# Optimization experiments

Measured on AMD Instinct MI355X. Metric: run time of the kernel, lower is better.

## Reference

```python
import jax, jax.numpy as jnp
import numpy as np

B, S, H = 2, 2048, 2048
HEADS, G = 16, 4
HD = H // HEADS          # 128
M = HEADS // G           # query heads per KV group


def setup_inputs() -> dict:
    key = jax.random.key(0)
    ks = jax.random.split(key, 6)
    s = 0.02
    hidden_state = jax.random.normal(ks[0], (B, S, H), dtype=jnp.float32)
    attention_mask = jnp.ones((B, 1, 1, S), dtype=jnp.float32)
    Wq = jax.random.normal(ks[1], (H, H), dtype=jnp.float32) * s
    bq = jnp.zeros((H,), dtype=jnp.float32)
    Wk = jax.random.normal(ks[2], (H, G * HD), dtype=jnp.float32) * s
    bk = jnp.zeros((G * HD,), dtype=jnp.float32)
    Wv = jax.random.normal(ks[3], (H, G * HD), dtype=jnp.float32) * s
    bv = jnp.zeros((G * HD,), dtype=jnp.float32)
    Wo = jax.random.normal(ks[4], (H, H), dtype=jnp.float32) * s
    bo = jnp.zeros((H,), dtype=jnp.float32)
    return {"hidden_state": hidden_state, "attention_mask": attention_mask,
            "Wq": Wq, "bq": bq, "Wk": Wk, "bk": bk, "Wv": Wv, "bv": bv,
            "Wo": Wo, "bo": bo}


def reference(hidden_state, attention_mask, Wq, bq, Wk, bk, Wv, bv, Wo, bo):
    b, s, h = hidden_state.shape
    # projections
    q = hidden_state @ Wq + bq                      # (B,S,H)
    k = hidden_state @ Wk + bk                      # (B,S,G*HD)
    v = hidden_state @ Wv + bv                      # (B,S,G*HD)
    # split heads; query head ordering is group-major (head = g*M + m),
    # matching the original expand/reshape of K/V groups.
    q = q.reshape(b, s, HEADS, HD).transpose(0, 2, 1, 3).reshape(b, G, M, s, HD)
    k = k.reshape(b, s, G, HD).transpose(0, 2, 1, 3)  # (B,G,S,HD)
    v = v.reshape(b, s, G, HD).transpose(0, 2, 1, 3)  # (B,G,S,HD)
    # grouped attention: avoid materializing expanded K/V
    scale = 1.0 / jnp.sqrt(jnp.float32(HD))
    scores = jnp.einsum('bgmqd,bgkd->bgmqk', q, k) * scale  # (B,G,M,S,S)
    # faithful to source: scores += mask * -1e-9 (mask shape (B,1,1,S))
    scores = scores + attention_mask[:, :, :, None, :] * (-1e-9)
    probs = jax.nn.softmax(scores, axis=-1)
    out = jnp.einsum('bgmqk,bgkd->bgmqd', probs, v)          # (B,G,M,S,HD)
    out = out.reshape(b, HEADS, s, HD).transpose(0, 2, 1, 3).reshape(b, s, h)
    return out @ Wo + bo
```

## Files before the change

kernel.cpp:

```cpp
#include <hip/hip_runtime.h>
#include <cstdint>

typedef unsigned short u16;
typedef __attribute__((ext_vector_type(8))) short bf16x8;
typedef __attribute__((ext_vector_type(4))) float f32x4;

#define B_    2
#define S_    2048
#define H_    2048
#define G_    4
#define HD_   128
#define QKVW  3072

#define EXP2F(x) __builtin_amdgcn_exp2f(x)

__device__ __forceinline__ u16 f2bf(float f) {
  union { float f; unsigned u; } v; v.f = f;
  unsigned r = v.u + 0x7fffu + ((v.u >> 16) & 1u);
  return (u16)(r >> 16);
}

__device__ __forceinline__ void async16(void* lds_dst, const void* gsrc) {
  __builtin_amdgcn_global_load_lds(
      (__attribute__((address_space(1))) void*)gsrc,
      (__attribute__((address_space(3))) void*)lds_dst, 16, 0, 0);
}

__global__ __launch_bounds__(256)
void prelude_kernel(const float* __restrict__ X, u16* __restrict__ Xb,
                    const float* __restrict__ Wq, const float* __restrict__ Wk,
                    const float* __restrict__ Wv, const float* __restrict__ Wo,
                    u16* __restrict__ Wqkvt, u16* __restrict__ Wot)
{
  int id = blockIdx.x;
  if (id < 4096) {
    int i = id * 256 + threadIdx.x;
    const float4* p = (const float4*)X + (size_t)i * 2;
    float4 a = p[0], b = p[1];
    u16 h[8] = { f2bf(a.x), f2bf(a.y), f2bf(a.z), f2bf(a.w),
                 f2bf(b.x), f2bf(b.y), f2bf(b.z), f2bf(b.w) };
    *(uint4*)(Xb + (size_t)i * 8) = *(const uint4*)h;
    return;
  }
  id -= 4096;
  const float* W; u16* Wt; int Ndim, bx;
  if (id < 4096)      { W = Wq; Wt = Wqkvt;                        Ndim = 2048; bx = id;        }
  else if (id < 5120) { W = Wk; Wt = Wqkvt + (size_t)2048 * 2048;  Ndim = 512;  bx = id - 4096; }
  else if (id < 6144) { W = Wv; Wt = Wqkvt + (size_t)2560 * 2048;  Ndim = 512;  bx = id - 5120; }
  else                { W = Wo; Wt = Wot;                          Ndim = 2048; bx = id - 6144; }
  const int Kdim = 2048;
  const int nbx = Ndim >> 5;
  const int n0 = (bx % nbx) * 32, k0 = (bx / nbx) * 32;

  __shared__ float t[32][33];
  int tx = threadIdx.x & 31, ty = threadIdx.x >> 5;
#pragma unroll
  for (int j = 0; j < 4; ++j)
    t[ty + j * 8][tx] = W[(size_t)(k0 + ty + j * 8) * Ndim + n0 + tx];
  __syncthreads();
#pragma unroll
  for (int j = 0; j < 4; ++j)
    Wt[(size_t)(n0 + ty + j * 8) * Kdim + k0 + tx] = f2bf(t[tx][ty + j * 8]);
}

__global__ __launch_bounds__(256)
void vtrans_kernel(const u16* __restrict__ Vb, u16* __restrict__ Vt)
{
  __shared__ u16 t[32][33];
  int tx = threadIdx.x & 31, ty = threadIdx.x >> 5;
  int s0 = blockIdx.x * 32, c0 = blockIdx.y * 32, b = blockIdx.z;
#pragma unroll
  for (int j = 0; j < 4; ++j)
    t[ty + j * 8][tx] = Vb[((size_t)(b * S_) + s0 + ty + j * 8) * QKVW + c0 + tx];
  __syncthreads();
#pragma unroll
  for (int j = 0; j < 4; ++j) {
    int c = c0 + ty + j * 8;
    int g = c >> 7, d = c & 127;
    Vt[(((size_t)(b * G_ + g)) * HD_ + d) * S_ + s0 + tx] = t[tx][ty + j * 8];
  }
}

template <int MODE>
__global__ __launch_bounds__(512, 6)
void gemm_bt(const u16* __restrict__ A, const u16* __restrict__ Bt,
             const float* __restrict__ biasQ, const float* __restrict__ biasK,
             const float* __restrict__ biasV, void* __restrict__ Cout,
             int Ndim, int Kdim)
{
  __shared__ u16 As[128 * 64];
  __shared__ u16 Bs[128 * 64];
  const int tid  = threadIdx.x;
  const int lane = tid & 63;
  const int wv   = tid >> 6;

  const int nwg  = gridDim.x * gridDim.y;
  const int wgid = blockIdx.x + gridDim.x * blockIdx.y;
  const int cpx  = nwg >> 3;
  const int swz  = (wgid & 7) * cpx + (wgid >> 3);
  const int row0 = (swz % gridDim.x) * 128;
  const int col0 = (swz / gridDim.x) * 128;

  const int wm = (wv >> 2) * 64;
  const int wn = (wv & 3) * 32;
  const int l15 = lane & 15, l4 = lane >> 4;

  f32x4 acc[4][2] = {};

  for (int kt = 0; kt < Kdim; kt += 64) {
    __syncthreads();
#pragma unroll
    for (int i = 0; i < 2; ++i) {
      int u = i * 512 + tid;
      int r = u >> 3, ci = u & 7;
      async16((char*)As + (i * 512 + wv * 64) * 16,
              A + (size_t)(row0 + r) * Kdim + kt + ci * 8);
    }
#pragma unroll
    for (int i = 0; i < 2; ++i) {
      int u = i * 512 + tid;
      int r = u >> 3, ci = u & 7;
      async16((char*)Bs + (i * 512 + wv * 64) * 16,
              Bt + (size_t)(col0 + r) * Kdim + kt + ci * 8);
    }
    __syncthreads();
#pragma unroll
    for (int ks = 0; ks < 2; ++ks) {
      bf16x8 af[4], bfr[2];
#pragma unroll
      for (int mt = 0; mt < 4; ++mt)
        af[mt] = *(const bf16x8*)&As[(wm + mt * 16 + l15) * 64 + ks * 32 + l4 * 8];
#pragma unroll
      for (int nt = 0; nt < 2; ++nt)
        bfr[nt] = *(const bf16x8*)&Bs[(wn + nt * 16 + l15) * 64 + ks * 32 + l4 * 8];
#pragma unroll
      for (int mt = 0; mt < 4; ++mt)
#pragma unroll
        for (int nt = 0; nt < 2; ++nt)
          acc[mt][nt] = __builtin_amdgcn_mfma_f32_16x16x32_bf16(af[mt], bfr[nt], acc[mt][nt], 0, 0, 0);
    }
  }

#pragma unroll
  for (int mt = 0; mt < 4; ++mt)
#pragma unroll
    for (int nt = 0; nt < 2; ++nt)
#pragma unroll
      for (int r = 0; r < 4; ++r) {
        int rr = row0 + wm + mt * 16 + l4 * 4 + r;
        int cc = col0 + wn + nt * 16 + l15;
        float bias;
        if (MODE == 3)
          bias = cc < 2048 ? biasQ[cc] : (cc < 2560 ? biasK[cc - 2048] : biasV[cc - 2560]);
        else
          bias = biasQ[cc];
        float v = acc[mt][nt][r] + bias;
        if (MODE == 3 && cc < 2048) v *= 0.12751743383412927f;
        if (MODE == 1) ((float*)Cout)[(size_t)rr * Ndim + cc] = v;
        else           ((u16*)Cout)[(size_t)rr * Ndim + cc] = f2bf(v);
      }
}

__global__ __launch_bounds__(512, 2)
void attn_kernel(const u16* __restrict__ Qb, const u16* __restrict__ Kb,
                 const u16* __restrict__ Vt, u16* __restrict__ Ob)
{
  __shared__ u16 SH[40960];
  u16* Ps = SH + 24576;
  const int tid  = threadIdx.x;
  const int lane = tid & 63, wv = tid >> 6;
  const int l15 = lane & 15, l4 = lane >> 4;
  const int qt = blockIdx.x, head = blockIdx.y, b = blockIdx.z;
  const int g = head >> 2;
  const int s0 = qt * 256;

  bf16x8 qf[2][4];
  {
    const u16* qbase = Qb + ((size_t)(b * S_ + s0 + wv * 32 + l15)) * QKVW + head * HD_ + l4 * 8;
#pragma unroll
    for (int rg = 0; rg < 2; ++rg)
#pragma unroll
      for (int ks = 0; ks < 4; ++ks)
        qf[rg][ks] = *(const bf16x8*)(qbase + (size_t)rg * 16 * QKVW + ks * 32);
  }

  float m_r[2][4], lp[2][4];
#pragma unroll
  for (int rg = 0; rg < 2; ++rg)
#pragma unroll
    for (int r = 0; r < 4; ++r) { m_r[rg][r] = 0.f; lp[rg][r] = 0.f; }
  f32x4 aco[2][8] = {};

#define STAGE_K(buf, kt_)                                                      \
  _Pragma("unroll")                                                            \
  for (int i = 0; i < 2; ++i) {                                                \
    int u = i * 512 + tid;                                                     \
    int r = u >> 4;                                                            \
    int ci = (u & 15) ^ (r & 7);                                               \
    async16((char*)SH + (buf) * 16384 + (i * 512 + wv * 64) * 16,              \
            Kb + ((size_t)(b * S_ + (kt_) * 64 + r)) * QKVW + g * HD_ + ci * 8); \
  }
#define STAGE_V(kt_)                                                           \
  _Pragma("unroll")                                                            \
  for (int i = 0; i < 2; ++i) {                                                \
    int u = i * 512 + tid;                                                     \
    int r = u >> 3;                                                            \
    int ci = (u & 7) ^ (r & 7);                                                \
    async16((char*)SH + 32768 + (i * 512 + wv * 64) * 16,                      \
            Vt + (((size_t)(b * G_ + g)) * HD_ + r) * S_ + (kt_) * 64 + ci * 8); \
  }

  STAGE_K(0, 0);
  STAGE_V(0);
  __syncthreads();

  const u16* Vc = SH + 16384;
  int kcur = 0;
  for (int kt = 0; kt < S_ / 64; ++kt) {
    if (kt + 1 < S_ / 64) {
      STAGE_K(kcur ^ 1, kt + 1);
    }
    const u16* Kc = SH + kcur * 8192;

    f32x4 sc[2][4] = {};
    __builtin_amdgcn_s_setprio(1);
#pragma unroll
    for (int ct = 0; ct < 4; ++ct)
#pragma unroll
      for (int ks = 0; ks < 4; ++ks) {
        bf16x8 kf = *(const bf16x8*)&Kc[(ct * 16 + l15) * 128 + ((ks * 32 + l4 * 8) ^ ((l15 & 7) << 3))];
        sc[0][ct] = __builtin_amdgcn_mfma_f32_16x16x32_bf16(qf[0][ks], kf, sc[0][ct], 0, 0, 0);
        sc[1][ct] = __builtin_amdgcn_mfma_f32_16x16x32_bf16(qf[1][ks], kf, sc[1][ct], 0, 0, 0);
      }
    __builtin_amdgcn_s_setprio(0);

    float lm[2][4];
    bool resc = false;
#pragma unroll
    for (int rg = 0; rg < 2; ++rg)
#pragma unroll
      for (int r = 0; r < 4; ++r) {
        lm[rg][r] = fmaxf(fmaxf(sc[rg][0][r], sc[rg][1][r]),
                          fmaxf(sc[rg][2][r], sc[rg][3][r]));
        float d = lm[rg][r] - m_r[rg][r];
        resc |= (d > 8.0f) | (d < -60.0f);
      }
    if (__ballot(resc)) {
#pragma unroll
      for (int rg = 0; rg < 2; ++rg)
#pragma unroll
        for (int r = 0; r < 4; ++r) {
          float mx = lm[rg][r];
          mx = fmaxf(mx, __shfl_xor(mx, 1));
          mx = fmaxf(mx, __shfl_xor(mx, 2));
          mx = fmaxf(mx, __shfl_xor(mx, 4));
          mx = fmaxf(mx, __shfl_xor(mx, 8));
          float mn = fmaxf(m_r[rg][r], mx);
          float al = EXP2F(m_r[rg][r] - mn);
          m_r[rg][r] = mn;
          lp[rg][r] *= al;
#pragma unroll
          for (int dt = 0; dt < 8; ++dt)
            aco[rg][dt][r] *= al;
        }
    }

#pragma unroll
    for (int rg = 0; rg < 2; ++rg)
#pragma unroll
      for (int ct = 0; ct < 4; ++ct)
#pragma unroll
        for (int r = 0; r < 4; ++r) {
          float p = EXP2F(sc[rg][ct][r] - m_r[rg][r]);
          lp[rg][r] += p;
          int row = wv * 32 + rg * 16 + l4 * 4 + r;
          int col = ct * 16 + l15;
          Ps[row * 64 + (((col >> 3) ^ (row & 7)) << 3) + (col & 7)] = f2bf(p);
        }

    __syncthreads();

    __builtin_amdgcn_s_setprio(1);
#pragma unroll
    for (int k2 = 0; k2 < 2; ++k2) {
      bf16x8 pa0, pa1;
      {
        int pr0 = wv * 32 + l15;
        int pr1 = wv * 32 + 16 + l15;
        pa0 = *(const bf16x8*)&Ps[pr0 * 64 + (((k2 * 4 + l4) ^ (pr0 & 7)) << 3)];
        pa1 = *(const bf16x8*)&Ps[pr1 * 64 + (((k2 * 4 + l4) ^ (pr1 & 7)) << 3)];
      }
#pragma unroll
      for (int dt = 0; dt < 8; ++dt) {
        bf16x8 vf = *(const bf16x8*)&Vc[(dt * 16 + l15) * 64 + ((k2 * 32 + l4 * 8) ^ ((l15 & 7) << 3))];
        aco[0][dt] = __builtin_amdgcn_mfma_f32_16x16x32_bf16(pa0, vf, aco[0][dt], 0, 0, 0);
        aco[1][dt] = __builtin_amdgcn_mfma_f32_16x16x32_bf16(pa1, vf, aco[1][dt], 0, 0, 0);
      }
    }
    __builtin_amdgcn_s_setprio(0);

    __syncthreads();
    if (kt + 1 < S_ / 64) {
      STAGE_V(kt + 1);
    }
    kcur ^= 1;
  }
#undef STAGE_K
#undef STAGE_V

#pragma unroll
  for (int rg = 0; rg < 2; ++rg)
#pragma unroll
    for (int r = 0; r < 4; ++r) {
      float s = lp[rg][r];
      s += __shfl_xor(s, 1);
      s += __shfl_xor(s, 2);
      s += __shfl_xor(s, 4);
      s += __shfl_xor(s, 8);
      lp[rg][r] = 1.0f / s;
    }
#pragma unroll
  for (int rg = 0; rg < 2; ++rg)
#pragma unroll
    for (int dt = 0; dt < 8; ++dt)
#pragma unroll
      for (int r = 0; r < 4; ++r) {
        int srow = s0 + wv * 32 + rg * 16 + l4 * 4 + r;
        int col = head * HD_ + dt * 16 + l15;
        Ob[((size_t)(b * S_ + srow)) * H_ + col] = f2bf(aco[rg][dt][r] * lp[rg][r]);
      }
}

extern "C" void kernel_launch(void* const* d_in, const int* in_sizes, int n_in,
                              void* d_out, int out_size, void* d_ws, size_t ws_size,
                              hipStream_t stream)
{
  const float* X    = (const float*)d_in[0];
  const float* Wq   = (const float*)d_in[2];
  const float* bq   = (const float*)d_in[3];
  const float* Wk   = (const float*)d_in[4];
  const float* bk   = (const float*)d_in[5];
  const float* Wv   = (const float*)d_in[6];
  const float* bv   = (const float*)d_in[7];
  const float* Wo   = (const float*)d_in[8];
  const float* bo   = (const float*)d_in[9];
  float* out = (float*)d_out;

  char* ws = (char*)d_ws;
  u16* Xb    = (u16*)(ws + 0);
  u16* QKV   = (u16*)(ws + (16u << 20));
  u16* Vt    = (u16*)(ws + (40u << 20));
  u16* Ab    = (u16*)(ws + (44u << 20));
  u16* Wqkvt = (u16*)(ws + (60u << 20));
  u16* Wot   = (u16*)(ws + (72u << 20));

  const u16* Qb = QKV;
  const u16* Kb = QKV + 2048;
  const u16* Vb = QKV + 2560;

  prelude_kernel<<<dim3(14336), 256, 0, stream>>>(X, Xb, Wq, Wk, Wv, Wo, Wqkvt, Wot);

  gemm_bt<3><<<dim3(32, 24), 512, 0, stream>>>(Xb, Wqkvt, bq, bk, bv, QKV, QKVW, 2048);

  vtrans_kernel<<<dim3(64, 16, 2), 256, 0, stream>>>(Vb, Vt);

  attn_kernel<<<dim3(8, 16, 2), 512, 0, stream>>>(Qb, Kb, Vt, Ab);

  gemm_bt<1><<<dim3(32, 16), 512, 0, stream>>>(Ab, Wot, bo, nullptr, nullptr, out, 2048, 2048);
}
```

Before: 248.0 us.

## Fuse V transpose into QKV GEMM epilogue and remap tiles per XCD

Removes the separate V transpose kernel by having the QKV GEMM epilogue write V columns directly into the transposed (B,G,HD,S) layout. The tile-to-workgroup swizzle is also changed to group row tiles per XCD. This saves a kernel launch and an extra read/write pass over V, but the transposed stores are strided 2-byte writes that coalesce poorly.

```diff
diff --git a/kernel.cpp b/kernel.cpp
--- a/kernel.cpp
+++ b/kernel.cpp
@@ -63,30 +63,12 @@
     Wt[(size_t)(n0 + ty + j * 8) * Kdim + k0 + tx] = f2bf(t[tx][ty + j * 8]);
 }
 
-__global__ __launch_bounds__(256)
-void vtrans_kernel(const u16* __restrict__ Vb, u16* __restrict__ Vt)
-{
-  __shared__ u16 t[32][33];
-  int tx = threadIdx.x & 31, ty = threadIdx.x >> 5;
-  int s0 = blockIdx.x * 32, c0 = blockIdx.y * 32, b = blockIdx.z;
-#pragma unroll
-  for (int j = 0; j < 4; ++j)
-    t[ty + j * 8][tx] = Vb[((size_t)(b * S_) + s0 + ty + j * 8) * QKVW + c0 + tx];
-  __syncthreads();
-#pragma unroll
-  for (int j = 0; j < 4; ++j) {
-    int c = c0 + ty + j * 8;
-    int g = c >> 7, d = c & 127;
-    Vt[(((size_t)(b * G_ + g)) * HD_ + d) * S_ + s0 + tx] = t[tx][ty + j * 8];
-  }
-}
-
 template <int MODE>
 __global__ __launch_bounds__(512, 6)
 void gemm_bt(const u16* __restrict__ A, const u16* __restrict__ Bt,
              const float* __restrict__ biasQ, const float* __restrict__ biasK,
              const float* __restrict__ biasV, void* __restrict__ Cout,
-             int Ndim, int Kdim)
+             u16* __restrict__ VtOut, int Ndim, int Kdim)
 {
   __shared__ u16 As[128 * 64];
   __shared__ u16 Bs[128 * 64];
@@ -94,12 +76,11 @@
   const int lane = tid & 63;
   const int wv   = tid >> 6;
 
-  const int nwg  = gridDim.x * gridDim.y;
   const int wgid = blockIdx.x + gridDim.x * blockIdx.y;
-  const int cpx  = nwg >> 3;
-  const int swz  = (wgid & 7) * cpx + (wgid >> 3);
-  const int row0 = (swz % gridDim.x) * 128;
-  const int col0 = (swz / gridDim.x) * 128;
+  const int xcd  = wgid & 7;
+  const int idx  = wgid >> 3;
+  const int row0 = (xcd * 4 + (idx & 3)) * 128;
+  const int col0 = (idx >> 2) * 128;
 
   const int wm = (wv >> 2) * 64;
   const int wn = (wv & 3) * 32;
@@ -155,9 +136,19 @@
         else
           bias = biasQ[cc];
         float v = acc[mt][nt][r] + bias;
-        if (MODE == 3 && cc < 2048) v *= 0.12751743383412927f;
-        if (MODE == 1) ((float*)Cout)[(size_t)rr * Ndim + cc] = v;
-        else           ((u16*)Cout)[(size_t)rr * Ndim + cc] = f2bf(v);
+        if (MODE == 1) {
+          ((float*)Cout)[(size_t)rr * Ndim + cc] = v;
+        } else {
+          if (cc < 2048) v *= 0.12751743383412927f;
+          if (cc < 2560) {
+            ((u16*)Cout)[(size_t)rr * Ndim + cc] = f2bf(v);
+          } else {
+            int vc = cc - 2560;
+            int gg = vc >> 7, d = vc & 127;
+            Vt_store:
+            VtOut[(((size_t)((rr >> 11) * G_ + gg)) * HD_ + d) * S_ + (rr & 2047)] = f2bf(v);
+          }
+        }
       }
 }
 
@@ -356,15 +347,12 @@
 
   const u16* Qb = QKV;
   const u16* Kb = QKV + 2048;
-  const u16* Vb = QKV + 2560;
 
   prelude_kernel<<<dim3(14336), 256, 0, stream>>>(X, Xb, Wq, Wk, Wv, Wo, Wqkvt, Wot);
 
-  gemm_bt<3><<<dim3(32, 24), 512, 0, stream>>>(Xb, Wqkvt, bq, bk, bv, QKV, QKVW, 2048);
-
-  vtrans_kernel<<<dim3(64, 16, 2), 256, 0, stream>>>(Vb, Vt);
+  gemm_bt<3><<<dim3(32, 24), 512, 0, stream>>>(Xb, Wqkvt, bq, bk, bv, QKV, Vt, QKVW, 2048);
 
   attn_kernel<<<dim3(8, 16, 2), 512, 0, stream>>>(Qb, Kb, Vt, Ab);
 
-  gemm_bt<1><<<dim3(32, 16), 512, 0, stream>>>(Ab, Wot, bo, nullptr, nullptr, out, 2048, 2048);
-}
+  gemm_bt<1><<<dim3(32, 16), 512, 0, stream>>>(Ab, Wot, bo, nullptr, nullptr, out, nullptr, 2048, 2048);
+}
```

After: 244.2 us. Within noise of the previous version (-1.5%).
